# Optimization experiments

Hardware: AMD Instinct MI355X
Metric: run time of the kernel (lower is better)

The kernel has to match this reference:

```python
import jax, jax.numpy as jnp
import numpy as np

N = 4096        # nodes
E = 65536       # edges (avg degree 16)
L = 64          # latent_dims
K = 256         # kernel_dims
ED = 6          # edge_dims
DEPTH = 2


def _gelu(x):
    # torch.nn.GELU / F.gelu default = exact erf form
    return jax.nn.gelu(x, approximate=False)


def setup_inputs() -> dict:
    key = jax.random.key(0)
    ks = jax.random.split(key, 12)
    u = lambda k, shape, fan: jax.random.uniform(k, shape, jnp.float32, -1.0, 1.0) / np.sqrt(fan)
    return {
        "nodes": jax.random.normal(ks[0], (N, L), jnp.float32),
        "edge_index": jax.random.randint(ks[1], (2, E), 0, N, jnp.int32),
        "edge_attr": jax.random.uniform(ks[2], (E, ED), jnp.float32),
        # DenseNet kernel MLP: ED -> K -> K -> L*L (GELU between layers)
        "W1": u(ks[3], (ED, K), ED), "b1": jnp.zeros((K,), jnp.float32),
        "W2": u(ks[4], (K, K), K),  "b2": jnp.zeros((K,), jnp.float32),
        "W3": u(ks[5], (K, L * L), K), "b3": jnp.zeros((L * L,), jnp.float32),
        # NNConv root linear (no bias) + conv bias
        "W_root": u(ks[6], (L, L), L),
        "bias": jnp.zeros((L,), jnp.float32),
    }


def reference(nodes, edge_index, edge_attr, W1, b1, W2, b2, W3, b3, W_root, bias):
    src, dst = edge_index[0], edge_index[1]
    # Edge-conditioned dynamic weights (depend only on edge_attr -> compute once)
    h = _gelu(edge_attr @ W1 + b1)          # [E, K]
    h = _gelu(h @ W2 + b2)                  # [E, K]
    W_edge = (h @ W3 + b3).reshape(E, L, L) # [E, L_in, L_out]

    def conv(x):
        msg = jnp.einsum('ei,eio->eo', x[src], W_edge)          # gather + per-edge matmul
        agg = jax.ops.segment_sum(msg, dst, num_segments=N)     # scatter-add to dst
        return agg + x @ W_root + bias

    x = nodes
    for idx in range(DEPTH):
        x = conv(x)
        if idx < DEPTH - 1:
            x = _gelu(x)
    return x
```

## Files before the change

kernel.cpp:

```cpp
#include <hip/hip_runtime.h>
#include <math.h>

#define NN 4096
#define NE 65536
#define LL 64
#define KK 256
#define ED 6
#define MAXSUPER 6144

typedef __bf16 bf16_t;
typedef __attribute__((ext_vector_type(4))) __bf16 bf16x4;
typedef __attribute__((ext_vector_type(8))) __bf16 bf16x8;
typedef __attribute__((ext_vector_type(4))) float f32x4;
typedef __attribute__((ext_vector_type(16))) float f32x16;

#define OFF_CNT    ((size_t)0)
#define OFF_DESC   ((size_t)16384)
#define OFF_AGG0   ((size_t)147456)
#define OFF_AGG1   ((size_t)1196032)
#define ZERO_BYTES ((size_t)2244608)
#define OFF_CURSOR ((size_t)2244608)
#define OFF_DSTS   ((size_t)2260992)
#define OFF_W2R    ((size_t)2785280)
#define OFF_W3RR   ((size_t)2916352)
#define OFF_Q0     ((size_t)5013504)
#define OFF_Q1     ((size_t)6062080)
#define OFF_X1F    ((size_t)7110656)
#define OFF_X0BF   ((size_t)8159232)
#define OFF_X1BF   ((size_t)8683520)
#define OFF_H      ((size_t)9207808)

__device__ __forceinline__ float gelu_f(float x) {
    return 0.5f * x * (1.0f + erff(x * 0.7071067811865476f));
}
__device__ __forceinline__ bf16_t f2bf(float x) { return (bf16_t)x; }

__global__ void k_hist(const int* __restrict__ ei, int* __restrict__ cnt) {
    int e = blockIdx.x * 256 + threadIdx.x;
    atomicAdd(&cnt[ei[e]], 1);
}

__global__ void k_scan(const int* __restrict__ cnt, int* __restrict__ cursor,
                       int4* __restrict__ descs) {
    __shared__ int pd[1024], pc[1024];
    int t = threadIdx.x;
    int deg[4]; int sd = 0, sc = 0;
#pragma unroll
    for (int j = 0; j < 4; j++) {
        deg[j] = cnt[t * 4 + j];
        sd += deg[j];
        sc += (deg[j] + 31) >> 5;
    }
    pd[t] = sd; pc[t] = sc;
    __syncthreads();
    for (int off = 1; off < 1024; off <<= 1) {
        int vd = 0, vc = 0;
        if (t >= off) { vd = pd[t - off]; vc = pc[t - off]; }
        __syncthreads();
        pd[t] += vd; pc[t] += vc;
        __syncthreads();
    }
    int rd = (t > 0) ? pd[t - 1] : 0;
    int rc = (t > 0) ? pc[t - 1] : 0;
    for (int j = 0; j < 4; j++) {
        int v = t * 4 + j, d = deg[j];
        cursor[v] = rd;
        int nch = (d + 31) >> 5;
        for (int c = 0; c < nch; c++) {
            int rem = d - c * 32;
            descs[rc + c] = make_int4(v, rd + c * 32, rem < 32 ? rem : 32, 0);
        }
        rc += nch; rd += d;
    }
}

__global__ void __launch_bounds__(256) k_fuse3(
        const int* __restrict__ ei, int* __restrict__ cursor, int* __restrict__ dsts,
        const float* __restrict__ W3, bf16_t* __restrict__ W3rr,
        const float* __restrict__ W2, bf16_t* __restrict__ W2r,
        const float* __restrict__ attr, const float* __restrict__ W1,
        const float* __restrict__ b1, bf16_t* __restrict__ a1,
        const float* __restrict__ x, const float* __restrict__ b3,
        bf16_t* __restrict__ xbf, float* __restrict__ Q) {
    __shared__ float smem[4096];
    int bid = blockIdx.x, tid = threadIdx.x;
    if (bid < 256) {
        int k0 = bid;
        for (int idx = tid; idx < 4096; idx += 256)
            smem[idx] = W3[(size_t)k0 * 4096 + idx];
        __syncthreads();
        int sbase = (2 * (k0 >> 4)) * 512 + (((k0 >> 3) & 1) * 32) * 8 + (k0 & 7);
#pragma unroll
        for (int m = 0; m < 2; m++) {
            int w = m * 256 + tid;
            int o = w >> 3, ib = w & 7;
            int s = sbase + (o >> 5) * 512 + (o & 31) * 8;
            int f = (s >> 4) * 1024 + (ib >> 2) * 512 + (ib & 3) * 128 + (s & 15) * 8;
            bf16x8 pk;
#pragma unroll
            for (int j = 0; j < 8; j++) pk[j] = f2bf(smem[(ib * 8 + j) * 64 + o]);
            *(bf16x8*)(W3rr + f) = pk;
        }
    } else if (bid < 512) {
        int t = (bid - 256) * 256 + tid;
        int kk = t >> 13, nn = (t >> 9) & 15, lane = (t >> 3) & 63, j = t & 7;
        int k = kk * 32 + (lane >> 4) * 8 + j;
        int n = nn * 16 + (lane & 15);
        W2r[t] = f2bf(W2[k * 256 + n]);
    } else if (bid < 1536) {
        float* sa = smem;
        int* spos = (int*)(smem + 512);
        int e0 = (bid - 512) * 64;
        for (int i = tid; i < 64 * ED; i += 256) sa[i] = attr[(size_t)e0 * ED + i];
        if (tid < 64) {
            int e = e0 + tid;
            int s = ei[e], d = ei[NE + e];
            int p = atomicAdd(&cursor[s], 1);
            dsts[p] = d;
            spos[tid] = p;
        }
        int col4 = (tid & 63) * 4;
        float w[ED][4], bb[4];
#pragma unroll
        for (int j = 0; j < ED; j++)
#pragma unroll
            for (int c = 0; c < 4; c++) w[j][c] = W1[j * 256 + col4 + c];
#pragma unroll
        for (int c = 0; c < 4; c++) bb[c] = b1[col4 + c];
        __syncthreads();
        int esub = tid >> 6;
#pragma unroll 1
        for (int eg = 0; eg < 16; eg++) {
            int el = eg * 4 + esub;
            int pos = spos[el];
            float av[ED];
#pragma unroll
            for (int j = 0; j < ED; j++) av[j] = sa[el * ED + j];
            bf16x4 ov;
#pragma unroll
            for (int c = 0; c < 4; c++) {
                float acc = bb[c];
#pragma unroll
                for (int j = 0; j < ED; j++) acc += av[j] * w[j][c];
                ov[c] = f2bf(gelu_f(acc));
            }
            *(bf16x4*)(a1 + (size_t)pos * 256 + col4) = ov;
        }
    } else {
        int v = (bid - 1536) * 4 + (tid >> 6);
        int o = tid & 63;
        float xv = x[v * 64 + o];
        smem[tid] = xv;
        xbf[v * 64 + o] = f2bf(xv);
        __syncthreads();
        const float* sx = smem + (tid >> 6) * 64;
        float q = 0.0f;
#pragma unroll 8
        for (int i = 0; i < 64; i++) q += sx[i] * b3[i * 64 + o];
        Q[v * 64 + o] = q;
    }
}

__global__ void __launch_bounds__(256) k_mlp2(const bf16_t* a1,
                                              const bf16_t* __restrict__ W2r,
                                              const float* __restrict__ b2,
                                              bf16_t* h) {
    __shared__ bf16_t sB[16384];
    int tid = threadIdx.x;
    int wave = tid >> 6, lane = tid & 63, col = lane & 15, quad = lane >> 4;
    int base = blockIdx.x * 128 + wave * 32;
    bf16x8 a[2][8];
#pragma unroll
    for (int t = 0; t < 2; t++) {
        const bf16_t* arow = a1 + (size_t)(base + t * 16 + col) * 256;
#pragma unroll
        for (int kk = 0; kk < 8; kk++)
            a[t][kk] = *(const bf16x8*)(arow + kk * 32 + quad * 8);
    }
#pragma unroll 1
    for (int p = 0; p < 4; p++) {
#pragma unroll
        for (int it = 0; it < 8; it++) {
            int c = it * 256 + tid;
            int fl = c >> 6;
            int e = (c & 63) * 8;
            int kk = fl >> 2, nnl = fl & 3;
            *(bf16x8*)(sB + fl * 512 + e) =
                *(const bf16x8*)(W2r + (size_t)(kk * 16 + p * 4 + nnl) * 512 + e);
        }
        __syncthreads();
#pragma unroll
        for (int nnl = 0; nnl < 4; nnl++) {
            f32x4 acc0, acc1;
#pragma unroll
            for (int r = 0; r < 4; r++) { acc0[r] = 0.0f; acc1[r] = 0.0f; }
#pragma unroll
            for (int kk = 0; kk < 8; kk++) {
                bf16x8 b = *(const bf16x8*)(sB + (kk * 4 + nnl) * 512 + lane * 8);
                acc0 = __builtin_amdgcn_mfma_f32_16x16x32_bf16(a[0][kk], b, acc0, 0, 0, 0);
                acc1 = __builtin_amdgcn_mfma_f32_16x16x32_bf16(a[1][kk], b, acc1, 0, 0, 0);
            }
            int ncol = (p * 4 + nnl) * 16 + col;
            float bv = b2[ncol];
#pragma unroll
            for (int r = 0; r < 4; r++) {
                int row0 = base + quad * 4 + r;
                h[(size_t)row0 * 256 + ncol] = f2bf(gelu_f(acc0[r] + bv));
                h[(size_t)(row0 + 16) * 256 + ncol] = f2bf(gelu_f(acc1[r] + bv));
            }
        }
        __syncthreads();
    }
}

__global__ void __launch_bounds__(512) k_fagg(const int4* __restrict__ descs,
                                              const int* __restrict__ dsts,
                                              const bf16_t* __restrict__ xbf,
                                              const bf16_t* __restrict__ W3rr,
                                              const bf16_t* __restrict__ h,
                                              const float* __restrict__ Q,
                                              float* __restrict__ agg) {
    __shared__ __align__(16) bf16_t Pls[4][16][264];
    __shared__ int sv[16], sbase[16], scnt[16];
    int tid = threadIdx.x, wave = tid >> 6, lane = tid & 63;
    if (tid < 16) {
        int4 d = descs[blockIdx.x * 16 + tid];
        sv[tid] = d.x; sbase[tid] = d.y; scnt[tid] = d.z;
    }
    __syncthreads();

    int col = lane & 15, quad = lane >> 4;
    int row = lane & 31, khalf = lane >> 5;

    const bf16_t* xr = xbf + (size_t)sv[col] * 64 + quad * 8;
    bf16x8 xa0 = *(const bf16x8*)xr;
    bf16x8 xa1 = *(const bf16x8*)(xr + 32);

    int s0 = wave * 2, s1 = s0 + 1;
    int v0 = sv[s0], v1 = sv[s1];
    int cnt0 = scnt[s0], cnt1 = scnt[s1];
    bool val0 = row < cnt0, val1 = row < cnt1;
    int pos0 = sbase[s0] + (val0 ? row : 0);
    int pos1 = sbase[s1] + (val1 ? row : 0);
    int dst0 = dsts[pos0], dst1 = dsts[pos1];
    const bf16_t* h0 = h + (size_t)pos0 * 256 + khalf * 8;
    const bf16_t* h1 = h + (size_t)pos1 * 256 + khalf * 8;

    bf16x8 zero;
#pragma unroll
    for (int i = 0; i < 8; i++) zero[i] = (bf16_t)0.0f;

    f32x16 acc00, acc01, acc10, acc11;
#pragma unroll
    for (int r = 0; r < 16; r++) { acc00[r] = 0.0f; acc01[r] = 0.0f;
                                   acc10[r] = 0.0f; acc11[r] = 0.0f; }

    int pst = wave >> 1;
    int nn0 = (wave & 1) * 8;

#pragma unroll 1
    for (int kt = 0; kt < 16; ++kt) {
        int strip = kt * 4 + pst;
        const bf16_t* wb = W3rr + (size_t)(strip * 16 + nn0) * 1024 + lane * 8;
#pragma unroll
        for (int nn = 0; nn < 8; ++nn) {
            bf16x8 b0 = *(const bf16x8*)wb;
            bf16x8 b1 = *(const bf16x8*)(wb + 512);
            wb += 1024;
            f32x4 acc;
#pragma unroll
            for (int r = 0; r < 4; r++) acc[r] = 0.0f;
            acc = __builtin_amdgcn_mfma_f32_16x16x32_bf16(b0, xa0, acc, 0, 0, 0);
            acc = __builtin_amdgcn_mfma_f32_16x16x32_bf16(b1, xa1, acc, 0, 0, 0);
            bf16x4 pk;
#pragma unroll
            for (int r = 0; r < 4; r++) pk[r] = f2bf(acc[r]);
            *(bf16x4*)(&Pls[pst][col][(nn0 + nn) * 16 + quad * 4]) = pk;
        }
        __syncthreads();
        {
            bf16x8 t0 = *(const bf16x8*)(h0 + kt * 16);
            bf16x8 af = val0 ? t0 : zero;
            bf16x8 pb0 = *(const bf16x8*)(&Pls[khalf][s0][row * 8]);
            bf16x8 pb1 = *(const bf16x8*)(&Pls[2 + khalf][s0][row * 8]);
            acc00 = __builtin_amdgcn_mfma_f32_32x32x16_bf16(af, pb0, acc00, 0, 0, 0);
            acc01 = __builtin_amdgcn_mfma_f32_32x32x16_bf16(af, pb1, acc01, 0, 0, 0);
        }
        {
            bf16x8 t1 = *(const bf16x8*)(h1 + kt * 16);
            bf16x8 af = val1 ? t1 : zero;
            bf16x8 pb0 = *(const bf16x8*)(&Pls[khalf][s1][row * 8]);
            bf16x8 pb1 = *(const bf16x8*)(&Pls[2 + khalf][s1][row * 8]);
            acc10 = __builtin_amdgcn_mfma_f32_32x32x16_bf16(af, pb0, acc10, 0, 0, 0);
            acc11 = __builtin_amdgcn_mfma_f32_32x32x16_bf16(af, pb1, acc11, 0, 0, 0);
        }
        __syncthreads();
    }

    {
        float q0 = Q[v0 * 64 + row];
        float q1 = Q[v0 * 64 + 32 + row];
#pragma unroll
        for (int r = 0; r < 16; r++) {
            int mm = (r & 3) + 8 * (r >> 2) + 4 * khalf;
            int de = __shfl(dst0, mm, 64);
            if (mm < cnt0) {
                atomicAdd(&agg[(size_t)de * 64 + row], acc00[r] + q0);
                atomicAdd(&agg[(size_t)de * 64 + 32 + row], acc01[r] + q1);
            }
        }
    }
    {
        float q0 = Q[v1 * 64 + row];
        float q1 = Q[v1 * 64 + 32 + row];
#pragma unroll
        for (int r = 0; r < 16; r++) {
            int mm = (r & 3) + 8 * (r >> 2) + 4 * khalf;
            int de = __shfl(dst1, mm, 64);
            if (mm < cnt1) {
                atomicAdd(&agg[(size_t)de * 64 + row], acc10[r] + q0);
                atomicAdd(&agg[(size_t)de * 64 + 32 + row], acc11[r] + q1);
            }
        }
    }
}

__global__ void k_combine1(const float* __restrict__ x, const float* __restrict__ agg,
                           const float* __restrict__ Wroot, const float* __restrict__ bias,
                           const float* __restrict__ b3, float* __restrict__ x1,
                           bf16_t* __restrict__ x1bf, float* __restrict__ Q1) {
    __shared__ float sx[64], sy[64];
    int v = blockIdx.x, o = threadIdx.x;
    sx[o] = x[v * 64 + o];
    __syncthreads();
    float acc = agg[v * 64 + o] + bias[o];
#pragma unroll 8
    for (int i = 0; i < 64; i++) acc += sx[i] * Wroot[i * 64 + o];
    acc = gelu_f(acc);
    x1[v * 64 + o] = acc;
    x1bf[v * 64 + o] = f2bf(acc);
    sy[o] = acc;
    __syncthreads();
    float q = 0.0f;
#pragma unroll 8
    for (int i = 0; i < 64; i++) q += sy[i] * b3[i * 64 + o];
    Q1[v * 64 + o] = q;
}

__global__ void k_combine2(const float* __restrict__ x1, const float* __restrict__ agg,
                           const float* __restrict__ Wroot, const float* __restrict__ bias,
                           float* __restrict__ out) {
    __shared__ float sx[64];
    int v = blockIdx.x, o = threadIdx.x;
    sx[o] = x1[v * 64 + o];
    __syncthreads();
    float acc = agg[v * 64 + o] + bias[o];
#pragma unroll 8
    for (int i = 0; i < 64; i++) acc += sx[i] * Wroot[i * 64 + o];
    out[v * 64 + o] = acc;
}

extern "C" void kernel_launch(void* const* d_in, const int* in_sizes, int n_in,
                              void* d_out, int out_size, void* d_ws, size_t ws_size,
                              hipStream_t stream) {
    const float* nodes = (const float*)d_in[0];
    const int*   ei    = (const int*)d_in[1];
    const float* attr  = (const float*)d_in[2];
    const float* W1    = (const float*)d_in[3];
    const float* b1    = (const float*)d_in[4];
    const float* W2    = (const float*)d_in[5];
    const float* b2    = (const float*)d_in[6];
    const float* W3    = (const float*)d_in[7];
    const float* b3    = (const float*)d_in[8];
    const float* Wroot = (const float*)d_in[9];
    const float* bias  = (const float*)d_in[10];
    float* out = (float*)d_out;
    char* ws = (char*)d_ws;

    int*    cnt    = (int*)(ws + OFF_CNT);
    int4*   descs  = (int4*)(ws + OFF_DESC);
    float*  agg0   = (float*)(ws + OFF_AGG0);
    float*  agg1   = (float*)(ws + OFF_AGG1);
    int*    cursor = (int*)(ws + OFF_CURSOR);
    int*    dsts   = (int*)(ws + OFF_DSTS);
    bf16_t* W2r    = (bf16_t*)(ws + OFF_W2R);
    bf16_t* W3rr   = (bf16_t*)(ws + OFF_W3RR);
    float*  Q0     = (float*)(ws + OFF_Q0);
    float*  Q1     = (float*)(ws + OFF_Q1);
    float*  x1f    = (float*)(ws + OFF_X1F);
    bf16_t* x0bf   = (bf16_t*)(ws + OFF_X0BF);
    bf16_t* x1bf   = (bf16_t*)(ws + OFF_X1BF);
    bf16_t* hbuf   = (bf16_t*)(ws + OFF_H);
    bf16_t* a1buf  = (bf16_t*)(ws + OFF_H);

    hipMemsetAsync(ws, 0, ZERO_BYTES, stream);
    k_hist<<<NE / 256, 256, 0, stream>>>(ei, cnt);
    k_scan<<<1, 1024, 0, stream>>>(cnt, cursor, descs);
    k_fuse3<<<2560, 256, 0, stream>>>(ei, cursor, dsts, W3, W3rr, W2, W2r,
                                      attr, W1, b1, a1buf, nodes, b3, x0bf, Q0);
    k_mlp2<<<512, 256, 0, stream>>>(a1buf, W2r, b2, hbuf);
    k_fagg<<<MAXSUPER / 16, 512, 0, stream>>>(descs, dsts, x0bf, W3rr, hbuf, Q0, agg0);
    k_combine1<<<NN, 64, 0, stream>>>(nodes, agg0, Wroot, bias, b3, x1f, x1bf, Q1);
    k_fagg<<<MAXSUPER / 16, 512, 0, stream>>>(descs, dsts, x1bf, W3rr, hbuf, Q1, agg1);
    k_combine2<<<NN, 64, 0, stream>>>(x1f, agg1, Wroot, bias, out);
}
```

Baseline: 284.7 us.

## Double-buffer P tiles and prefetch W3/h loads in fused aggregation kernel

```diff
diff --git a/kernel.cpp b/kernel.cpp
--- a/kernel.cpp
+++ b/kernel.cpp
@@ -220,7 +220,7 @@
                                               const bf16_t* __restrict__ h,
                                               const float* __restrict__ Q,
                                               float* __restrict__ agg) {
-    __shared__ __align__(16) bf16_t Pls[4][16][264];
+    __shared__ __align__(16) bf16_t Pls[2][4][16][264];
     __shared__ int sv[16], sbase[16], scnt[16];
     int tid = threadIdx.x, wave = tid >> 6, lane = tid & 63;
     if (tid < 16) {
@@ -228,6 +228,11 @@
         sv[tid] = d.x; sbase[tid] = d.y; scnt[tid] = d.z;
     }
     __syncthreads();
+
+    int tot = 0;
+#pragma unroll
+    for (int i = 0; i < 16; i++) tot |= scnt[i];
+    if (tot == 0) return;
 
     int col = lane & 15, quad = lane >> 4;
     int row = lane & 31, khalf = lane >> 5;
@@ -258,43 +263,80 @@
     int pst = wave >> 1;
     int nn0 = (wave & 1) * 8;
 
-#pragma unroll 1
+    bf16x8 wA[8], wB[8];
+    bf16x8 hc0, hc1;
+
+    {
+        const bf16_t* wb = W3rr + (size_t)((0 * 4 + pst) * 16 + nn0) * 1024 + lane * 8;
+#pragma unroll
+        for (int nn = 0; nn < 8; ++nn) {
+            wA[nn] = *(const bf16x8*)wb;
+            wB[nn] = *(const bf16x8*)(wb + 512);
+            wb += 1024;
+        }
+        hc0 = *(const bf16x8*)h0;
+        hc1 = *(const bf16x8*)h1;
+#pragma unroll
+        for (int nn = 0; nn < 8; ++nn) {
+            f32x4 acc;
+#pragma unroll
+            for (int r = 0; r < 4; r++) acc[r] = 0.0f;
+            acc = __builtin_amdgcn_mfma_f32_16x16x32_bf16(wA[nn], xa0, acc, 0, 0, 0);
+            acc = __builtin_amdgcn_mfma_f32_16x16x32_bf16(wB[nn], xa1, acc, 0, 0, 0);
+            bf16x4 pk;
+#pragma unroll
+            for (int r = 0; r < 4; r++) pk[r] = f2bf(acc[r]);
+            *(bf16x4*)(&Pls[0][pst][col][(nn0 + nn) * 16 + quad * 4]) = pk;
+        }
+    }
+    __syncthreads();
+
+#pragma unroll 2
     for (int kt = 0; kt < 16; ++kt) {
-        int strip = kt * 4 + pst;
-        const bf16_t* wb = W3rr + (size_t)(strip * 16 + nn0) * 1024 + lane * 8;
-#pragma unroll
-        for (int nn = 0; nn < 8; ++nn) {
-            bf16x8 b0 = *(const bf16x8*)wb;
-            bf16x8 b1 = *(const bf16x8*)(wb + 512);
-            wb += 1024;
-            f32x4 acc;
-#pragma unroll
-            for (int r = 0; r < 4; r++) acc[r] = 0.0f;
-            acc = __builtin_amdgcn_mfma_f32_16x16x32_bf16(b0, xa0, acc, 0, 0, 0);
-            acc = __builtin_amdgcn_mfma_f32_16x16x32_bf16(b1, xa1, acc, 0, 0, 0);
-            bf16x4 pk;
-#pragma unroll
-            for (int r = 0; r < 4; r++) pk[r] = f2bf(acc[r]);
-            *(bf16x4*)(&Pls[pst][col][(nn0 + nn) * 16 + quad * 4]) = pk;
-        }
-        __syncthreads();
+        int cur = kt & 1, nxt = cur ^ 1;
+        bf16x8 hn0, hn1;
+        if (kt < 15) {
+            const bf16_t* wb = W3rr + (size_t)(((kt + 1) * 4 + pst) * 16 + nn0) * 1024
+                               + lane * 8;
+#pragma unroll
+            for (int nn = 0; nn < 8; ++nn) {
+                wA[nn] = *(const bf16x8*)wb;
+                wB[nn] = *(const bf16x8*)(wb + 512);
+                wb += 1024;
+            }
+            hn0 = *(const bf16x8*)(h0 + (kt + 1) * 16);
+            hn1 = *(const bf16x8*)(h1 + (kt + 1) * 16);
+        }
         {
-            bf16x8 t0 = *(const bf16x8*)(h0 + kt * 16);
-            bf16x8 af = val0 ? t0 : zero;
-            bf16x8 pb0 = *(const bf16x8*)(&Pls[khalf][s0][row * 8]);
-            bf16x8 pb1 = *(const bf16x8*)(&Pls[2 + khalf][s0][row * 8]);
+            bf16x8 af = val0 ? hc0 : zero;
+            bf16x8 pb0 = *(const bf16x8*)(&Pls[cur][khalf][s0][row * 8]);
+            bf16x8 pb1 = *(const bf16x8*)(&Pls[cur][2 + khalf][s0][row * 8]);
             acc00 = __builtin_amdgcn_mfma_f32_32x32x16_bf16(af, pb0, acc00, 0, 0, 0);
             acc01 = __builtin_amdgcn_mfma_f32_32x32x16_bf16(af, pb1, acc01, 0, 0, 0);
         }
         {
-            bf16x8 t1 = *(const bf16x8*)(h1 + kt * 16);
-            bf16x8 af = val1 ? t1 : zero;
-            bf16x8 pb0 = *(const bf16x8*)(&Pls[khalf][s1][row * 8]);
-            bf16x8 pb1 = *(const bf16x8*)(&Pls[2 + khalf][s1][row * 8]);
+            bf16x8 af = val1 ? hc1 : zero;
+            bf16x8 pb0 = *(const bf16x8*)(&Pls[cur][khalf][s1][row * 8]);
+            bf16x8 pb1 = *(const bf16x8*)(&Pls[cur][2 + khalf][s1][row * 8]);
             acc10 = __builtin_amdgcn_mfma_f32_32x32x16_bf16(af, pb0, acc10, 0, 0, 0);
             acc11 = __builtin_amdgcn_mfma_f32_32x32x16_bf16(af, pb1, acc11, 0, 0, 0);
         }
-        __syncthreads();
+        if (kt < 15) {
+#pragma unroll
+            for (int nn = 0; nn < 8; ++nn) {
+                f32x4 acc;
+#pragma unroll
+                for (int r = 0; r < 4; r++) acc[r] = 0.0f;
+                acc = __builtin_amdgcn_mfma_f32_16x16x32_bf16(wA[nn], xa0, acc, 0, 0, 0);
+                acc = __builtin_amdgcn_mfma_f32_16x16x32_bf16(wB[nn], xa1, acc, 0, 0, 0);
+                bf16x4 pk;
+#pragma unroll
+                for (int r = 0; r < 4; r++) pk[r] = f2bf(acc[r]);
+                *(bf16x4*)(&Pls[nxt][pst][col][(nn0 + nn) * 16 + quad * 4]) = pk;
+            }
+            hc0 = hn0; hc1 = hn1;
+            __syncthreads();
+        }
     }
 
     {
```

Result: slower. 296.8 us (+4.2%).
